# Kernel tuning notes

Hardware: AMD Instinct MI355X
Metric: run time of the kernel (lower is better)

The kernel has to match this reference:

```python
import jax, jax.numpy as jnp
import numpy as np

B, S, D_IN, D_OUT = 4, 8192, 1024, 1024


def setup_inputs() -> dict:
    key = jax.random.key(0)
    k1, k2, k3, k4 = jax.random.split(key, 4)
    x = jax.random.normal(k1, (B, S, D_IN), dtype=jnp.float32)
    # signed int8 weights, stored int8 as in the torch buffer
    weight_int = jax.random.randint(k2, (D_OUT, D_IN), -128, 128, dtype=jnp.int32).astype(jnp.int8)
    # realistic per-output-channel scales
    weight_scale = jax.random.uniform(k3, (D_OUT,), dtype=jnp.float32, minval=0.005, maxval=0.02)
    input_scale = jnp.asarray(0.05, dtype=jnp.float32)
    bias = jax.random.normal(k4, (D_OUT,), dtype=jnp.float32) * 0.01
    return {"x": x, "weight_int": weight_int, "weight_scale": weight_scale,
            "input_scale": input_scale, "bias": bias}


def reference(x, weight_int, weight_scale, input_scale, bias):
    # quantize activations to int8 (faithful: round, clamp, cast)
    x_int = jnp.clip(jnp.round(x / input_scale), -128, 127).astype(jnp.int8)
    # module upcasts both operands to fp32 for the matmul
    out = jnp.matmul(x_int.astype(jnp.float32), weight_int.astype(jnp.float32).T)
    # dequantize: per-output-channel weight scale * scalar input scale, then bias
    out = out * weight_scale * input_scale + bias
    return out
```

## Files before the change

kernel.cpp:

```cpp
#include <hip/hip_runtime.h>
#include <stdint.h>
#include <stddef.h>

typedef int   v4i __attribute__((ext_vector_type(4)));
typedef float v4f __attribute__((ext_vector_type(4)));

#define M_DIM 32768
#define N_DIM 1024
#define K_DIM 1024
#define BM 64
#define KSTEPS 16

__global__ __launch_bounds__(256)
void repack_w_kernel(const int* __restrict__ w32, int* __restrict__ wf)
{
    const int i  = blockIdx.x * 256 + threadIdx.x;
    const int f  = i >> 8;
    const int r  = i & 255;
    const int ln = r >> 2;
    const int dw = r & 3;
    const int j  = f & 3;
    const int ks = (f >> 2) & 15;
    const int wv = (f >> 6) & 7;
    const int np = f >> 9;
    const int n  = np * 512 + wv * 64 + j * 16 + (ln & 15);
    const int k  = ks * 64 + (ln >> 4) * 16 + dw * 4;
    const v4i v  = *(const v4i*)&w32[(size_t)n * K_DIM + k];
    wf[i] = (v[0] & 255) | ((v[1] & 255) << 8) |
            ((v[2] & 255) << 16) | ((v[3] & 255) << 24);
}

__global__ __launch_bounds__(512, 4)
void fused_kernel(const float* __restrict__ x,
                  const signed char* __restrict__ Wf,
                  const float* __restrict__ wscale,
                  const float* __restrict__ iscale_p,
                  const float* __restrict__ bias,
                  float* __restrict__ out)
{
    __shared__ signed char lA[BM * K_DIM];

    const int mrow0 = blockIdx.x * BM;
    const int t  = threadIdx.x;
    const int wv = t >> 6;
    const int ln = t & 63;

    {
        const float inv = 1.0f / *iscale_p;
        const int colf = (t & 255) * 4;
        const int rsub = t >> 8;
        for (int j = 0; j < 32; ++j) {
            const int row = j * 2 + rsub;
            const v4f v = *(const v4f*)&x[(size_t)(mrow0 + row) * K_DIM + colf];
            int r = 0;
            #pragma unroll
            for (int e = 0; e < 4; ++e) {
                float q = rintf(v[e] * inv);
                q = fminf(127.f, fmaxf(-128.f, q));
                r |= ((int)q & 255) << (8 * e);
            }
            *(int*)&lA[row * K_DIM + (colf ^ ((row & 7) << 4))] = r;
        }
    }
    __syncthreads();

    const int lr = ln & 15;
    const int kh = (ln >> 4) * 16;
    const float is = *iscale_p;

    for (int np = 0; np < 2; ++np) {
        v4i acc[4][4] = {};
        #pragma unroll 4
        for (int ks = 0; ks < KSTEPS; ++ks) {
            v4i aF[4], bF[4];
            #pragma unroll
            for (int i = 0; i < 4; ++i) {
                const int row = i * 16 + lr;
                aF[i] = *(const v4i*)&lA[row * K_DIM +
                                         ((ks * 64 + kh) ^ ((row & 7) << 4))];
            }
            const size_t fbase = ((size_t)(np * 8 + wv) * 16 + ks) * 4;
            #pragma unroll
            for (int j = 0; j < 4; ++j)
                bF[j] = *(const v4i*)&Wf[(fbase + j) * 1024 + ln * 16];
            #pragma unroll
            for (int i = 0; i < 4; ++i)
                #pragma unroll
                for (int j = 0; j < 4; ++j)
                    acc[i][j] = __builtin_amdgcn_mfma_i32_16x16x64_i8(
                                    bF[j], aF[i], acc[i][j], 0, 0, 0);
        }
        #pragma unroll
        for (int j = 0; j < 4; ++j) {
            const int nb = np * 512 + wv * 64 + j * 16 + ((ln >> 4) << 2);
            v4f sc4 = *(const v4f*)&wscale[nb];
            const v4f bv4 = *(const v4f*)&bias[nb];
            sc4 *= is;
            #pragma unroll
            for (int i = 0; i < 4; ++i) {
                const int m = mrow0 + i * 16 + lr;
                v4f o;
                #pragma unroll
                for (int r = 0; r < 4; ++r)
                    o[r] = (float)acc[i][j][r] * sc4[r] + bv4[r];
                *(v4f*)&out[(size_t)m * N_DIM + nb] = o;
            }
        }
    }
}

extern "C" void kernel_launch(void* const* d_in, const int* in_sizes, int n_in,
                              void* d_out, int out_size, void* d_ws, size_t ws_size,
                              hipStream_t stream)
{
    const float* x       = (const float*)d_in[0];
    const int*   w32     = (const int*)d_in[1];
    const float* wscale  = (const float*)d_in[2];
    const float* iscale  = (const float*)d_in[3];
    const float* bias    = (const float*)d_in[4];
    float* out           = (float*)d_out;

    signed char* wf = (signed char*)d_ws;

    repack_w_kernel<<<(N_DIM * K_DIM / 4) / 256, 256, 0, stream>>>(w32, (int*)wf);

    fused_kernel<<<M_DIM / BM, 512, 0, stream>>>(x, wf, wscale, iscale, bias, out);
}
```

Baseline: 71.21 us.

## Switch to 32x32x32 int8 MFMA with double-buffered weight fragment prefetch

Replaces the 16x16x64 int8 MFMA tiling with 32x32x32 MFMAs, and changes the weight repack layout to match the new fragment shape. The two N-halves are merged into a single 32-step loop. Weight fragments for the next step are prefetched into alternating register buffers so global loads overlap with the MFMAs. This aims to cut LDS reads per MFMA and hide weight load latency, at the cost of a more complex loop and possibly higher register pressure under the 4-blocks launch bound.

```diff
diff --git a/kernel.cpp b/kernel.cpp
--- a/kernel.cpp
+++ b/kernel.cpp
@@ -2,8 +2,9 @@
 #include <stdint.h>
 #include <stddef.h>
 
-typedef int   v4i __attribute__((ext_vector_type(4)));
-typedef float v4f __attribute__((ext_vector_type(4)));
+typedef int   v4i  __attribute__((ext_vector_type(4)));
+typedef int   v16i __attribute__((ext_vector_type(16)));
+typedef float v4f  __attribute__((ext_vector_type(4)));
 
 #define M_DIM 32768
 #define N_DIM 1024
@@ -19,12 +20,13 @@
     const int r  = i & 255;
     const int ln = r >> 2;
     const int dw = r & 3;
-    const int j  = f & 3;
-    const int ks = (f >> 2) & 15;
-    const int wv = (f >> 6) & 7;
-    const int np = f >> 9;
-    const int n  = np * 512 + wv * 64 + j * 16 + (ln & 15);
-    const int k  = ks * 64 + (ln >> 4) * 16 + dw * 4;
+    const int j    = f & 1;
+    const int ksub = (f >> 1) & 1;
+    const int ks   = (f >> 2) & 15;
+    const int wv   = (f >> 6) & 7;
+    const int np   = f >> 9;
+    const int n  = np * 512 + wv * 64 + j * 32 + (ln & 31);
+    const int k  = ks * 64 + ksub * 32 + (ln >> 5) * 16 + dw * 4;
     const v4i v  = *(const v4i*)&w32[(size_t)n * K_DIM + k];
     wf[i] = (v[0] & 255) | ((v[1] & 255) << 8) |
             ((v[2] & 255) << 16) | ((v[3] & 255) << 24);
@@ -44,6 +46,8 @@
     const int t  = threadIdx.x;
     const int wv = t >> 6;
     const int ln = t & 63;
+    const int lm = ln & 31;
+    const int kq = (ln >> 5) * 16;
 
     {
         const float inv = 1.0f / *iscale_p;
@@ -64,49 +68,86 @@
     }
     __syncthreads();
 
-    const int lr = ln & 15;
-    const int kh = (ln >> 4) * 16;
     const float is = *iscale_p;
 
-    for (int np = 0; np < 2; ++np) {
-        v4i acc[4][4] = {};
-        #pragma unroll 4
-        for (int ks = 0; ks < KSTEPS; ++ks) {
-            v4i aF[4], bF[4];
+    #define FBASE(u) ((((size_t)(u >> 4) * 8 + wv) * 16 + (u & 15)) * 4)
+
+    v4i bC[4], bN[4];
+    #pragma unroll
+    for (int q = 0; q < 4; ++q)
+        bC[q] = *(const v4i*)&Wf[(FBASE(0) + q) * 1024 + ln * 16];
+
+    v16i acc[2][2] = {};
+    #pragma unroll 2
+    for (int u = 0; u < 32; ++u) {
+        const int np = u >> 4;
+        const int ks = u & 15;
+        const int un = (u + 1 < 32) ? u + 1 : 31;
+        if ((u & 1) == 0) {
             #pragma unroll
-            for (int i = 0; i < 4; ++i) {
-                const int row = i * 16 + lr;
-                aF[i] = *(const v4i*)&lA[row * K_DIM +
-                                         ((ks * 64 + kh) ^ ((row & 7) << 4))];
-            }
-            const size_t fbase = ((size_t)(np * 8 + wv) * 16 + ks) * 4;
+            for (int q = 0; q < 4; ++q)
+                bN[q] = *(const v4i*)&Wf[(FBASE(un) + q) * 1024 + ln * 16];
+        } else {
             #pragma unroll
-            for (int j = 0; j < 4; ++j)
-                bF[j] = *(const v4i*)&Wf[(fbase + j) * 1024 + ln * 16];
+            for (int q = 0; q < 4; ++q)
+                bC[q] = *(const v4i*)&Wf[(FBASE(un) + q) * 1024 + ln * 16];
+        }
+        v4i aF[2][2];
+        #pragma unroll
+        for (int i = 0; i < 2; ++i) {
+            const int row = i * 32 + lm;
             #pragma unroll
-            for (int i = 0; i < 4; ++i)
+            for (int s = 0; s < 2; ++s)
+                aF[i][s] = *(const v4i*)&lA[row * K_DIM +
+                             ((ks * 64 + s * 32 + kq) ^ ((row & 7) << 4))];
+        }
+        if ((u & 1) == 0) {
+            #pragma unroll
+            for (int i = 0; i < 2; ++i)
                 #pragma unroll
-                for (int j = 0; j < 4; ++j)
-                    acc[i][j] = __builtin_amdgcn_mfma_i32_16x16x64_i8(
-                                    bF[j], aF[i], acc[i][j], 0, 0, 0);
+                for (int j = 0; j < 2; ++j)
+                    #pragma unroll
+                    for (int s = 0; s < 2; ++s)
+                        acc[i][j] = __builtin_amdgcn_mfma_i32_32x32x32_i8(
+                                        bC[s * 2 + j], aF[i][s], acc[i][j], 0, 0, 0);
+        } else {
+            #pragma unroll
+            for (int i = 0; i < 2; ++i)
+                #pragma unroll
+                for (int j = 0; j < 2; ++j)
+                    #pragma unroll
+                    for (int s = 0; s < 2; ++s)
+                        acc[i][j] = __builtin_amdgcn_mfma_i32_32x32x32_i8(
+                                        bN[s * 2 + j], aF[i][s], acc[i][j], 0, 0, 0);
         }
-        #pragma unroll
-        for (int j = 0; j < 4; ++j) {
-            const int nb = np * 512 + wv * 64 + j * 16 + ((ln >> 4) << 2);
-            v4f sc4 = *(const v4f*)&wscale[nb];
-            const v4f bv4 = *(const v4f*)&bias[nb];
-            sc4 *= is;
+        if (ks == 15) {
             #pragma unroll
-            for (int i = 0; i < 4; ++i) {
-                const int m = mrow0 + i * 16 + lr;
-                v4f o;
+            for (int j = 0; j < 2; ++j)
                 #pragma unroll
-                for (int r = 0; r < 4; ++r)
-                    o[r] = (float)acc[i][j][r] * sc4[r] + bv4[r];
-                *(v4f*)&out[(size_t)m * N_DIM + nb] = o;
-            }
+                for (int q = 0; q < 4; ++q) {
+                    const int nb = np * 512 + wv * 64 + j * 32 + q * 8 +
+                                   ((ln >> 5) << 2);
+                    v4f sc4 = *(const v4f*)&wscale[nb];
+                    const v4f bv4 = *(const v4f*)&bias[nb];
+                    sc4 *= is;
+                    #pragma unroll
+                    for (int i = 0; i < 2; ++i) {
+                        const int m = mrow0 + i * 32 + lm;
+                        v4f o;
+                        #pragma unroll
+                        for (int r = 0; r < 4; ++r)
+                            o[r] = (float)acc[i][j][q * 4 + r] * sc4[r] + bv4[r];
+                        *(v4f*)&out[(size_t)m * N_DIM + nb] = o;
+                    }
+                }
+            #pragma unroll
+            for (int i = 0; i < 2; ++i)
+                #pragma unroll
+                for (int j = 0; j < 2; ++j)
+                    acc[i][j] = (v16i)(0);
         }
     }
+    #undef FBASE
 }
 
 extern "C" void kernel_launch(void* const* d_in, const int* in_sizes, int n_in,
```

New measurement: 92.26 us. 29.6% more time.
